# Optimization experiments

Hardware: AMD Instinct MI355X
Metric: run time of the kernel (lower is better)

Reference implementation:

```python
import jax, jax.numpy as jnp
import numpy as np

TEMPERATURE = 0.1
EPS = 1e-12


def _normalize(x):
    # torch F.normalize(dim=-1): x / max(||x||_2, eps)
    n = jnp.sqrt(jnp.sum(x * x, axis=-1, keepdims=True))
    return x / jnp.maximum(n, EPS)


def setup_inputs() -> dict:
    key = jax.random.key(0)
    k1, k2, k3 = jax.random.split(key, 3)
    b, p, d = 64, 196, 256
    return {
        "batch_tokens1": jax.random.normal(k1, (b, p, d), dtype=jnp.float32),
        "batch_tokens2": jax.random.normal(k2, (b, p, d), dtype=jnp.float32),
        "labels": jax.random.randint(k3, (b, 1), 0, 4),
        "epoch": 100,
    }


def reference(batch_tokens1, batch_tokens2, labels, epoch):
    t1 = _normalize(batch_tokens1)  # [b, p, d]
    t2 = _normalize(batch_tokens2)
    b, p, d = t1.shape

    # (b*p) x (b*p) token-wise similarity, then [b1, b2, p1, p2]
    sim = jnp.einsum('ki,mi->km', t1.reshape(b * p, d), t2.reshape(b * p, d))
    sim = sim.reshape(b, p, b, p).transpose(0, 2, 1, 3)  # [b1, b2, p1, p2]

    # max over p2 for 1->2, max over p1 for 2->1; then mean over remaining patch dim
    max12 = jnp.max(sim, axis=-1)      # [b1, b2, p1]
    idx12 = jnp.argmax(sim, axis=-1)   # [b1, b2, p1]
    sim_1_to_2 = jnp.mean(max12, axis=-1)  # [b1, b2]

    idx21 = jnp.argmax(sim, axis=-2)   # [b1, b2, p2]

    diag = jnp.arange(b)
    idx_to_keep1_2 = idx12[diag, diag]  # [b, p] (diagonal over b1==b2)
    idx_to_keep2_1 = idx21[diag, diag]  # [b, p]

    # cross-entropy of sim_1_to_2/T against targets arange(b), mean reduction
    logits = sim_1_to_2 / TEMPERATURE
    loss = jnp.mean(jax.nn.logsumexp(logits, axis=-1) - logits[diag, diag])
    return loss, idx_to_keep1_2, idx_to_keep2_1
```

## Files before the change

### kernel.cpp

```cpp
#include <hip/hip_runtime.h>
#include <math.h>

#define NB 64
#define NP 196
#define ND 256
#define NBP (NB * NP)

typedef __bf16 v8bf __attribute__((ext_vector_type(8)));
typedef float f32x16 __attribute__((ext_vector_type(16)));
typedef int v8i __attribute__((ext_vector_type(8)));

#define WS_T1Q    116736
#define WS_T2Q    3328000
#define WS_PARTS  7522304
#define WS_NEED   7923712

__device__ __forceinline__ unsigned int fmono(float v) {
    unsigned int u = __float_as_uint(v);
    return (u & 0x80000000u) ? ~u : (u | 0x80000000u);
}
__device__ __forceinline__ unsigned long long packVI(float v, int idx) {
    return ((unsigned long long)fmono(v) << 32) | (unsigned int)(~idx);
}

__device__ __forceinline__ v8i mkop(int4 lo, int4 hi) {
    v8i r;
    r[0] = lo.x; r[1] = lo.y; r[2] = lo.z; r[3] = lo.w;
    r[4] = hi.x; r[5] = hi.y; r[6] = hi.z; r[7] = hi.w;
    return r;
}


__global__ __launch_bounds__(256)
void filip_prep8(const float* __restrict__ t1, const float* __restrict__ t2,
                 float* __restrict__ inv1, float* __restrict__ inv2,
                 float* __restrict__ sim12,
                 char* __restrict__ t1q, char* __restrict__ t2q) {
    const int tid = threadIdx.x;
    if (blockIdx.x == 0) {
        float4 z = make_float4(0.f, 0.f, 0.f, 0.f);
        float4* s4 = reinterpret_cast<float4*>(sim12);
        #pragma unroll
        for (int j = 0; j < 4; ++j) s4[tid * 4 + j] = z;
    }
    int id = blockIdx.x * 4 + (tid >> 6);
    int L = tid & 63;
    int chunk = L >> 4, hi = (L >> 3) & 1, half = (L >> 2) & 1, j0 = (L & 3) * 4;
    if (id < NBP) {
        const float* src = t1 + (size_t)id * ND;
        float4 v = reinterpret_cast<const float4*>(src)[L];
        float ss = v.x * v.x + v.y * v.y + v.z * v.z + v.w * v.w;
        #pragma unroll
        for (int off = 32; off > 0; off >>= 1) ss += __shfl_xor(ss, off, 64);
        float inv = 1.0f / fmaxf(sqrtf(ss), 1e-12f);
        if (L == 0) inv1[id] = inv;
        int w0 = __builtin_amdgcn_cvt_pk_fp8_f32(v.x * inv, v.y * inv, 0, false);
        int w  = __builtin_amdgcn_cvt_pk_fp8_f32(v.z * inv, v.w * inv, w0, true);
        int t = id >> 7, r = id & 127;
        *reinterpret_cast<int*>(t1q + (size_t)t * 32768 + chunk * 8192 + hi * 4096
                                + half * 2048 + r * 16 + j0) = w;
    } else {
        int pid = id - NBP;
        int b2 = pid >> 8, c = pid & 255;
        char* dst = t2q + (size_t)b2 * 65536 + chunk * 16384 + hi * 8192
                    + half * 4096 + c * 16 + j0;
        if (c < NP) {
            const float* src = t2 + (size_t)(b2 * NP + c) * ND;
            float4 v = reinterpret_cast<const float4*>(src)[L];
            float ss = v.x * v.x + v.y * v.y + v.z * v.z + v.w * v.w;
            #pragma unroll
            for (int off = 32; off > 0; off >>= 1) ss += __shfl_xor(ss, off, 64);
            float inv = 1.0f / fmaxf(sqrtf(ss), 1e-12f);
            if (L == 0) inv2[b2 * NP + c] = inv;
            int w0 = __builtin_amdgcn_cvt_pk_fp8_f32(v.x * inv, v.y * inv, 0, false);
            int w  = __builtin_amdgcn_cvt_pk_fp8_f32(v.z * inv, v.w * inv, w0, true);
            *reinterpret_cast<int*>(dst) = w;
        } else {
            *reinterpret_cast<int*>(dst) = 0;
        }
    }
}

#define BM 128
#define BN 256

#define LOADA(TOFF)                                                          \
    _Pragma("unroll")                                                        \
    for (int c = 0; c < 4; ++c)                                              \
        _Pragma("unroll")                                                    \
        for (int mt = 0; mt < 2; ++mt) {                                     \
            const char* p = Ag + (TOFF) + c * 8192 + mt * 512;               \
            int4 lo = *reinterpret_cast<const int4*>(p);                     \
            int4 h4 = *reinterpret_cast<const int4*>(p + 2048);              \
            aA[c][mt] = mkop(lo, h4);                                        \
        }

#define ZEROACC                                                              \
    _Pragma("unroll")                                                        \
    for (int mt = 0; mt < 2; ++mt)                                           \
        _Pragma("unroll")                                                    \
        for (int nt = 0; nt < 4; ++nt)                                       \
            _Pragma("unroll")                                                \
            for (int r = 0; r < 16; ++r) acc[mt][nt][r] = 0.0f;

#define KLOOP                                                                \
    __builtin_amdgcn_s_setprio(1);                                           \
    _Pragma("unroll")                                                        \
    for (int c = 0; c < 4; ++c) {                                            \
        v8i bfr[4];                                                          \
        _Pragma("unroll")                                                    \
        for (int nt = 0; nt < 4; ++nt) {                                     \
            const char* p = Bl + c * 16384 + nt * 512;                       \
            int4 lo = *reinterpret_cast<const int4*>(p);                     \
            int4 h4 = *reinterpret_cast<const int4*>(p + 4096);              \
            bfr[nt] = mkop(lo, h4);                                          \
        }                                                                    \
        _Pragma("unroll")                                                    \
        for (int mt = 0; mt < 2; ++mt)                                       \
            _Pragma("unroll")                                                \
            for (int nt = 0; nt < 4; ++nt)                                   \
                acc[mt][nt] = __builtin_amdgcn_mfma_scale_f32_32x32x64_f8f6f4(\
                    aA[c][mt], bfr[nt], acc[mt][nt], 0, 0, 0, 127u, 0, 127u);\
    }                                                                        \
    __builtin_amdgcn_s_setprio(0);

#define FOLDRM(RM)                                                           \
    _Pragma("unroll")                                                        \
    for (int mt = 0; mt < 2; ++mt)                                           \
        _Pragma("unroll")                                                    \
        for (int r = 0; r < 16; ++r)                                         \
            RM[mt][r] = fmaxf(fmaxf(acc[mt][0][r], acc[mt][1][r]),           \
                              fmaxf(acc[mt][2][r], acc[mt][3][r]));

#define EPILOG(RM, BROW)                                                     \
    _Pragma("unroll")                                                        \
    for (int mt = 0; mt < 2; ++mt) {                                         \
        _Pragma("unroll")                                                    \
        for (int r = 0; r < 16; ++r) {                                       \
            int row = wr * 64 + mt * 32 + (r & 3) + 8 * (r >> 2) + 4 * hi;   \
            pmx[row][wc * 32 + ln] = RM[mt][r];                              \
        }                                                                    \
    }                                                                        \
    __syncthreads();                                                         \
    if (tid < BM) {                                                          \
        const float4* prow = reinterpret_cast<const float4*>(pmx[tid]);      \
        float m = -3.0e38f;                                                  \
        _Pragma("unroll")                                                    \
        for (int j = 0; j < 16; ++j) {                                       \
            float4 v = prow[j];                                              \
            m = fmaxf(m, fmaxf(fmaxf(v.x, v.y), fmaxf(v.z, v.w)));           \
        }                                                                    \
        int grow = (BROW) * BM + tid;                                        \
        int b1 = grow / NP;                                                  \
        int fb = ((BROW) * BM) / NP;                                         \
        float v0 = (b1 == fb) ? m : 0.0f;                                    \
        float v1 = (b1 != fb) ? m : 0.0f;                                    \
        _Pragma("unroll")                                                    \
        for (int off = 1; off < 64; off <<= 1) {                             \
            v0 += __shfl_xor(v0, off, 64);                                   \
            v1 += __shfl_xor(v1, off, 64);                                   \
        }                                                                    \
        if (lane == 0) {                                                     \
            atomicAdd(&sim12[fb * NB + b2], v0);                             \
            int lb = ((BROW) * BM + BM - 1) / NP;                            \
            if (lb != fb) atomicAdd(&sim12[lb * NB + b2], v1);               \
        }                                                                    \
    }                                                                        \
    __syncthreads();

__global__ __launch_bounds__(256, 2)
void filip_mega(const char* __restrict__ t1q, const char* __restrict__ t2q,
                float* __restrict__ sim12,
                const float* __restrict__ t1, const float* __restrict__ t2,
                const float* __restrict__ inv1, const float* __restrict__ inv2,
                unsigned long long* __restrict__ parts,
                float* __restrict__ out)
{
    __shared__ __align__(16) char smem[65536];
    const int bid = blockIdx.x;
    const int tid = threadIdx.x;

    if (bid >= 256) {
        int n = bid - 256;
        int x = n & 7, local = n >> 3;
        const int pairT = local >> 3;
        const int b2    = x * 8 + (local & 7);

        const int lane = tid & 63, wave = tid >> 6;
        const int wr = wave >> 1, wc = wave & 1;
        const int ln = lane & 31, hi = lane >> 5;

        const char* Ag = t1q + (size_t)(pairT * 2) * 32768
                       + hi * 4096 + (wr * 64 + ln) * 16;
        const char* Bg = t2q + (size_t)b2 * 65536;

        v8i aA[4][2];
        LOADA(0)

        #pragma unroll
        for (int i = 0; i < 16; ++i) {
            *reinterpret_cast<ulonglong2*>(smem + i * 4096 + tid * 16) =
                *reinterpret_cast<const ulonglong2*>(Bg + i * 4096 + tid * 16);
        }

        f32x16 acc[2][4];
        ZEROACC
        __syncthreads();

        const char* Bl = smem + hi * 8192 + wc * 2048 + ln * 16;
        float rm0[2][16], rm1[2][16];

        KLOOP
        FOLDRM(rm0)

        LOADA(32768)
        ZEROACC
        KLOOP
        FOLDRM(rm1)

        __syncthreads();

        float (*pmx)[68] = reinterpret_cast<float (*)[68]>(smem);
        EPILOG(rm0, pairT * 2)
        EPILOG(rm1, pairT * 2 + 1)
        return;
    }

    {
        const int q = bid & 3;
        const int b = bid >> 2;
        const int r0 = q * 49;
        const int tx = tid & 15, ty = tid >> 4;

        float* As = reinterpret_cast<float*>(smem);
        float* Bs = As + 2176;
        unsigned long long* colP = reinterpret_cast<unsigned long long*>(smem);

        const float* Ap = t1 + (size_t)b * NP * ND;
        const float* Bp = t2 + (size_t)b * NP * ND;
        const float* ia = inv1 + b * NP;
        const float* ib = inv2 + b * NP;

        float acc[4][4][4];
        #pragma unroll
        for (int i = 0; i < 4; ++i)
            #pragma unroll
            for (int j = 0; j < 4; ++j)
                #pragma unroll
                for (int l = 0; l < 4; ++l) acc[i][j][l] = 0.0f;

        for (int kc = 0; kc < 8; ++kc) {
            __syncthreads();
            #pragma unroll
            for (int i = 0; i < 2; ++i) {
                int f4 = tid + 256 * i;
                int row = f4 >> 3, k4 = f4 & 7;
                float4 v = make_float4(0.f, 0.f, 0.f, 0.f);
                if (row < 49) {
                    v = *reinterpret_cast<const float4*>(Ap + (size_t)(r0 + row) * ND + kc * 32 + 4 * k4);
                    float s = ia[r0 + row];
                    v.x *= s; v.y *= s; v.z *= s; v.w *= s;
                }
                As[(4 * k4 + 0) * 68 + row] = v.x;
                As[(4 * k4 + 1) * 68 + row] = v.y;
                As[(4 * k4 + 2) * 68 + row] = v.z;
                As[(4 * k4 + 3) * 68 + row] = v.w;
            }
            #pragma unroll
            for (int i = 0; i < 8; ++i) {
                int f4 = tid + 256 * i;
                int col = f4 >> 3, k4 = f4 & 7;
                float4 v = make_float4(0.f, 0.f, 0.f, 0.f);
                if (col < NP) {
                    v = *reinterpret_cast<const float4*>(Bp + (size_t)col * ND + kc * 32 + 4 * k4);
                    float s = ib[col];
                    v.x *= s; v.y *= s; v.z *= s; v.w *= s;
                }
                Bs[(4 * k4 + 0) * 260 + col] = v.x;
                Bs[(4 * k4 + 1) * 260 + col] = v.y;
                Bs[(4 * k4 + 2) * 260 + col] = v.z;
                Bs[(4 * k4 + 3) * 260 + col] = v.w;
            }
            __syncthreads();
            #pragma unroll 4
            for (int k = 0; k < 32; ++k) {
                float a0 = As[k * 68 + 4 * ty + 0];
                float a1 = As[k * 68 + 4 * ty + 1];
                float a2 = As[k * 68 + 4 * ty + 2];
                float a3 = As[k * 68 + 4 * ty + 3];
                float4 bq[4];
                #pragma unroll
                for (int j = 0; j < 4; ++j)
                    bq[j] = *reinterpret_cast<const float4*>(&Bs[k * 260 + 4 * tx + 64 * j]);
                #pragma unroll
                for (int j = 0; j < 4; ++j) {
                    acc[0][j][0] = fmaf(a0, bq[j].x, acc[0][j][0]);
                    acc[0][j][1] = fmaf(a0, bq[j].y, acc[0][j][1]);
                    acc[0][j][2] = fmaf(a0, bq[j].z, acc[0][j][2]);
                    acc[0][j][3] = fmaf(a0, bq[j].w, acc[0][j][3]);
                    acc[1][j][0] = fmaf(a1, bq[j].x, acc[1][j][0]);
                    acc[1][j][1] = fmaf(a1, bq[j].y, acc[1][j][1]);
                    acc[1][j][2] = fmaf(a1, bq[j].z, acc[1][j][2]);
                    acc[1][j][3] = fmaf(a1, bq[j].w, acc[1][j][3]);
                    acc[2][j][0] = fmaf(a2, bq[j].x, acc[2][j][0]);
                    acc[2][j][1] = fmaf(a2, bq[j].y, acc[2][j][1]);
                    acc[2][j][2] = fmaf(a2, bq[j].z, acc[2][j][2]);
                    acc[2][j][3] = fmaf(a2, bq[j].w, acc[2][j][3]);
                    acc[3][j][0] = fmaf(a3, bq[j].x, acc[3][j][0]);
                    acc[3][j][1] = fmaf(a3, bq[j].y, acc[3][j][1]);
                    acc[3][j][2] = fmaf(a3, bq[j].z, acc[3][j][2]);
                    acc[3][j][3] = fmaf(a3, bq[j].w, acc[3][j][3]);
                }
            }
        }

        #pragma unroll
        for (int i = 0; i < 4; ++i) {
            unsigned long long best = 0ull;
            #pragma unroll
            for (int j = 0; j < 4; ++j)
                #pragma unroll
                for (int l = 0; l < 4; ++l) {
                    int c = 64 * j + 4 * tx + l;
                    if (c < NP) {
                        unsigned long long p = packVI(acc[i][j][l], c);
                        if (p > best) best = p;
                    }
                }
            #pragma unroll
            for (int off = 1; off < 16; off <<= 1) {
                unsigned long long o = __shfl_xor(best, off, 16);
                if (o > best) best = o;
            }
            int rl = 4 * ty + i;
            if (tx == 0 && rl < 49)
                out[1 + b * NP + r0 + rl] = (float)(unsigned int)(~best);
        }

        __syncthreads();
        #pragma unroll
        for (int j = 0; j < 4; ++j)
            #pragma unroll
            for (int l = 0; l < 4; ++l) {
                unsigned long long best = 0ull;
                #pragma unroll
                for (int i = 0; i < 4; ++i) {
                    int rl = 4 * ty + i;
                    if (rl < 49) {
                        unsigned long long p = packVI(acc[i][j][l], r0 + rl);
                        if (p > best) best = p;
                    }
                }
                colP[ty * 256 + 64 * j + 4 * tx + l] = best;
            }
        __syncthreads();
        {
            unsigned long long best = 0ull;
            #pragma unroll
            for (int y = 0; y < 16; ++y) {
                unsigned long long o = colP[y * 256 + tid];
                if (o > best) best = o;
            }
            if (tid < NP) parts[(b * 4 + q) * NP + tid] = best;
        }
    }
}

__global__ void filip_finloss(const unsigned long long* __restrict__ parts,
                              const float* __restrict__ sim12,
                              float* __restrict__ out) {
    if (blockIdx.x < 49) {
        int id = blockIdx.x * 256 + threadIdx.x;
        int b = id / NP, c = id - b * NP;
        unsigned long long best = 0ull;
        #pragma unroll
        for (int qq = 0; qq < 4; ++qq) {
            unsigned long long o = parts[(b * 4 + qq) * NP + c];
            if (o > best) best = o;
        }
        out[1 + NBP + id] = (float)(unsigned int)(~best);
    } else if (threadIdx.x < 64) {
        int i = threadIdx.x;
        const float SC = 10.0f / 196.0f;
        const float* row = sim12 + i * NB;
        float mx = -3.0e38f;
        for (int j = 0; j < NB; ++j) mx = fmaxf(mx, row[j] * SC);
        float s = 0.0f;
        for (int j = 0; j < NB; ++j) s += expf(row[j] * SC - mx);
        float lse = mx + logf(s);
        float li = lse - row[i] * SC;
        #pragma unroll
        for (int off = 32; off > 0; off >>= 1)
            li += __shfl_xor(li, off, 64);
        if (i == 0) out[0] = li / 64.0f;
    }
}

__global__ void filip_norms(const float* __restrict__ t1,
                            const float* __restrict__ t2,
                            float* __restrict__ inv1,
                            float* __restrict__ inv2,
                            float* __restrict__ sim12) {
    int row = blockIdx.x;
    int lane = threadIdx.x;
    if (row < NB) sim12[row * NB + lane] = 0.0f;
    const float* src; float* dst; int r;
    if (row < NBP) { src = t1; dst = inv1; r = row; }
    else           { src = t2; dst = inv2; r = row - NBP; }
    float4 v = reinterpret_cast<const float4*>(src + (size_t)r * ND)[lane];
    float ss = v.x * v.x + v.y * v.y + v.z * v.z + v.w * v.w;
    #pragma unroll
    for (int off = 32; off > 0; off >>= 1)
        ss += __shfl_xor(ss, off, 64);
    if (lane == 0)
        dst[r] = 1.0f / fmaxf(sqrtf(ss), 1e-12f);
}

__device__ __forceinline__ v8bf cvt8(float4 a, float4 b, float s) {
    v8bf v;
    v[0] = (__bf16)(a.x * s); v[1] = (__bf16)(a.y * s);
    v[2] = (__bf16)(a.z * s); v[3] = (__bf16)(a.w * s);
    v[4] = (__bf16)(b.x * s); v[5] = (__bf16)(b.y * s);
    v[6] = (__bf16)(b.z * s); v[7] = (__bf16)(b.w * s);
    return v;
}

#define BKF 64
__global__ __launch_bounds__(256, 2)
void filip_mfma(const float* __restrict__ t1, const float* __restrict__ t2,
                const float* __restrict__ inv1, const float* __restrict__ inv2,
                float* __restrict__ sim12)
{
    __shared__ unsigned short Asb[BM * BKF];
    __shared__ unsigned short Bsb[BN * BKF];
    __shared__ float rmx[2][BM];

    const int bRow = blockIdx.x;
    const int b2   = blockIdx.y;
    const int tid  = threadIdx.x;
    const int lane = tid & 63, wave = tid >> 6;
    const int wr = wave >> 1, wc = wave & 1;
    const int ln = lane & 31, hi = lane >> 5;

    const float* Abase = t1 + (size_t)bRow * BM * ND;
    const float* Bbase = t2 + (size_t)b2 * NP * ND;

    f32x16 acc[2][4];
    #pragma unroll
    for (int mt = 0; mt < 2; ++mt)
        #pragma unroll
        for (int nt = 0; nt < 4; ++nt)
            #pragma unroll
            for (int r = 0; r < 16; ++r) acc[mt][nt][r] = 0.0f;

    for (int kc = 0; kc < 4; ++kc) {
        __syncthreads();
        #pragma unroll
        for (int i = 0; i < 4; ++i) {
            int flat = (i * 256 + tid) * 8;
            int r = flat >> 6, k0 = flat & 63;
            const float* gp = Abase + (size_t)r * ND + kc * BKF + k0;
            float4 f0 = *reinterpret_cast<const float4*>(gp);
            float4 f1 = *reinterpret_cast<const float4*>(gp + 4);
            float s = inv1[bRow * BM + r];
            v8bf v = cvt8(f0, f1, s);
            int off = r * 128 + ((k0 * 2) ^ ((r & 7) << 4));
            *reinterpret_cast<v8bf*>(reinterpret_cast<char*>(Asb) + off) = v;
        }
        #pragma unroll
        for (int i = 0; i < 8; ++i) {
            int flat = (i * 256 + tid) * 8;
            int r = flat >> 6, k0 = flat & 63;
            v8bf v;
            if (r < NP) {
                const float* gp = Bbase + (size_t)r * ND + kc * BKF + k0;
                float4 f0 = *reinterpret_cast<const float4*>(gp);
                float4 f1 = *reinterpret_cast<const float4*>(gp + 4);
                float s = inv2[b2 * NP + r];
                v = cvt8(f0, f1, s);
            } else {
                #pragma unroll
                for (int j = 0; j < 8; ++j) v[j] = (__bf16)0.0f;
            }
            int off = r * 128 + ((k0 * 2) ^ ((r & 7) << 4));
            *reinterpret_cast<v8bf*>(reinterpret_cast<char*>(Bsb) + off) = v;
        }
        __syncthreads();
        #pragma unroll
        for (int ks = 0; ks < 4; ++ks) {
            const int kb = ks * 32 + hi * 16;
            v8bf af[2], bfr[4];
            #pragma unroll
            for (int mt = 0; mt < 2; ++mt) {
                int r = wr * 64 + mt * 32 + ln;
                af[mt] = *reinterpret_cast<const v8bf*>(
                    reinterpret_cast<const char*>(Asb) + r * 128 + (kb ^ ((r & 7) << 4)));
            }
            #pragma unroll
            for (int nt = 0; nt < 4; ++nt) {
                int c = wc * 128 + nt * 32 + ln;
                bfr[nt] = *reinterpret_cast<const v8bf*>(
                    reinterpret_cast<const char*>(Bsb) + c * 128 + (kb ^ ((c & 7) << 4)));
            }
            #pragma unroll
            for (int mt = 0; mt < 2; ++mt)
                #pragma unroll
                for (int nt = 0; nt < 4; ++nt)
                    acc[mt][nt] = __builtin_amdgcn_mfma_f32_32x32x16_bf16(
                        af[mt], bfr[nt], acc[mt][nt], 0, 0, 0);
        }
    }

    #pragma unroll
    for (int mt = 0; mt < 2; ++mt) {
        float t[16];
        #pragma unroll
        for (int r = 0; r < 16; ++r) {
            float m = fmaxf(fmaxf(acc[mt][0][r], acc[mt][1][r]),
                            fmaxf(acc[mt][2][r], acc[mt][3][r]));
            #pragma unroll
            for (int off = 1; off <= 16; off <<= 1)
                m = fmaxf(m, __shfl_xor(m, off, 64));
            t[r] = m;
        }
        if (ln == 0) {
            #pragma unroll
            for (int r = 0; r < 16; ++r) {
                int row = wr * 64 + mt * 32 + (r & 3) + 8 * (r >> 2) + 4 * hi;
                rmx[wc][row] = t[r];
            }
        }
    }
    __syncthreads();
    if (tid < BM) {
        float m = fmaxf(rmx[0][tid], rmx[1][tid]);
        int grow = bRow * BM + tid;
        int b1 = grow / NP;
        int fb = (bRow * BM) / NP;
        float v0 = (b1 == fb) ? m : 0.0f;
        float v1 = (b1 != fb) ? m : 0.0f;
        #pragma unroll
        for (int off = 1; off < 64; off <<= 1) {
            v0 += __shfl_xor(v0, off, 64);
            v1 += __shfl_xor(v1, off, 64);
        }
        if (lane == 0) {
            atomicAdd(&sim12[fb * NB + b2], v0);
            int lb = (bRow * BM + BM - 1) / NP;
            if (lb != fb) atomicAdd(&sim12[lb * NB + b2], v1);
        }
    }
}

__global__ __launch_bounds__(256)
void filip_diag(const float* __restrict__ t1, const float* __restrict__ t2,
                const float* __restrict__ inv1, const float* __restrict__ inv2,
                float* __restrict__ out)
{
    const int b = blockIdx.x;
    const int tid = threadIdx.x;
    const int tx = tid & 15, ty = tid >> 4;

    __shared__ float As2[16][209];
    __shared__ float Bs2[16][65];
    __shared__ float colV[16][65];
    __shared__ int   colI[16][65];

    const float* Ap = t1 + (size_t)b * NP * ND;
    const float* Bp = t2 + (size_t)b * NP * ND;
    const float* ia = inv1 + b * NP;
    const float* ib = inv2 + b * NP;

    float rmax[13];
    int   ridx[13];
    #pragma unroll
    for (int m = 0; m < 13; ++m) { rmax[m] = -3.0e38f; ridx[m] = 1 << 30; }

    for (int tile = 0; tile < 4; ++tile) {
        float acc[13][4];
        #pragma unroll
        for (int m = 0; m < 13; ++m)
            #pragma unroll
            for (int n = 0; n < 4; ++n) acc[m][n] = 0.0f;

        for (int kk = 0; kk < 16; ++kk) {
            __syncthreads();
            #pragma unroll
            for (int i = 0; i < 13; ++i) {
                int e = tid + 256 * i;
                int p1 = e >> 4, k = e & 15;
                float v = 0.0f;
                if (p1 < NP) v = Ap[p1 * ND + kk * 16 + k] * ia[p1];
                As2[k][p1] = v;
            }
            #pragma unroll
            for (int i = 0; i < 4; ++i) {
                int e = tid + 256 * i;
                int pl = e >> 4, k = e & 15;
                int p2 = tile * 64 + pl;
                float v = 0.0f;
                if (p2 < NP) v = Bp[p2 * ND + kk * 16 + k] * ib[p2];
                Bs2[k][pl] = v;
            }
            __syncthreads();
            #pragma unroll 4
            for (int k = 0; k < 16; ++k) {
                float a[13], bq[4];
                #pragma unroll
                for (int m = 0; m < 13; ++m) a[m] = As2[k][ty + 16 * m];
                #pragma unroll
                for (int n = 0; n < 4; ++n) bq[n] = Bs2[k][tx + 16 * n];
                #pragma unroll
                for (int m = 0; m < 13; ++m)
                    #pragma unroll
                    for (int n = 0; n < 4; ++n)
                        acc[m][n] = fmaf(a[m], bq[n], acc[m][n]);
            }
        }

        #pragma unroll
        for (int n = 0; n < 4; ++n) {
            int c = tile * 64 + tx + 16 * n;
            if (c < NP) {
                #pragma unroll
                for (int m = 0; m < 13; ++m) {
                    float v = acc[m][n];
                    if (v > rmax[m] || (v == rmax[m] && c < ridx[m])) {
                        rmax[m] = v; ridx[m] = c;
                    }
                }
            }
        }

        #pragma unroll
        for (int n = 0; n < 4; ++n) {
            float bv = -3.0e38f; int bi = 1 << 30;
            #pragma unroll
            for (int m = 0; m < 13; ++m) {
                int row = ty + 16 * m;
                if (row < NP) {
                    float v = acc[m][n];
                    if (v > bv || (v == bv && row < bi)) { bv = v; bi = row; }
                }
            }
            colV[ty][tx + 16 * n] = bv;
            colI[ty][tx + 16 * n] = bi;
        }
        __syncthreads();
        if (tid < 64) {
            int c = tile * 64 + tid;
            if (c < NP) {
                float bv = -3.0e38f; int bi = 1 << 30;
                #pragma unroll
                for (int y = 0; y < 16; ++y) {
                    float v = colV[y][tid]; int i2 = colI[y][tid];
                    if (v > bv || (v == bv && i2 < bi)) { bv = v; bi = i2; }
                }
                out[1 + NBP + b * NP + c] = (float)bi;
            }
        }
        __syncthreads();
    }

    #pragma unroll
    for (int m = 0; m < 13; ++m) {
        float v = rmax[m]; int ix = ridx[m];
        #pragma unroll
        for (int off = 1; off < 16; off <<= 1) {
            float ov = __shfl_xor(v, off, 16);
            int   oi = __shfl_xor(ix, off, 16);
            if (ov > v || (ov == v && oi < ix)) { v = ov; ix = oi; }
        }
        rmax[m] = v; ridx[m] = ix;
    }
    if (tx == 0) {
        #pragma unroll
        for (int m = 0; m < 13; ++m) {
            int row = ty + 16 * m;
            if (row < NP) out[1 + b * NP + row] = (float)ridx[m];
        }
    }
}

__global__ void filip_loss(const float* __restrict__ sim12,
                           float* __restrict__ out) {
    int i = threadIdx.x;
    const float SC = 10.0f / 196.0f;
    const float* row = sim12 + i * NB;
    float mx = -3.0e38f;
    for (int j = 0; j < NB; ++j) mx = fmaxf(mx, row[j] * SC);
    float s = 0.0f;
    for (int j = 0; j < NB; ++j) s += expf(row[j] * SC - mx);
    float lse = mx + logf(s);
    float li = lse - row[i] * SC;
    #pragma unroll
    for (int off = 32; off > 0; off >>= 1)
        li += __shfl_xor(li, off, 64);
    if (i == 0) out[0] = li / 64.0f;
}

extern "C" void kernel_launch(void* const* d_in, const int* in_sizes, int n_in,
                              void* d_out, int out_size, void* d_ws, size_t ws_size,
                              hipStream_t stream) {
    const float* t1 = (const float*)d_in[0];
    const float* t2 = (const float*)d_in[1];
    float* out = (float*)d_out;
    float* ws  = (float*)d_ws;

    float* inv1  = ws;
    float* inv2  = ws + NBP;
    float* sim12 = ws + 2 * NBP;

    if (ws_size >= (size_t)WS_NEED) {
        char* t1q = (char*)d_ws + WS_T1Q;
        char* t2q = (char*)d_ws + WS_T2Q;
        unsigned long long* parts = (unsigned long long*)((char*)d_ws + WS_PARTS);

        filip_prep8<<<(NBP + NB * 256) / 4, 256, 0, stream>>>(t1, t2, inv1, inv2, sim12, t1q, t2q);
        filip_mega<<<256 + 3136, 256, 0, stream>>>(t1q, t2q, sim12, t1, t2, inv1, inv2, parts, out);
        filip_finloss<<<50, 256, 0, stream>>>(parts, sim12, out);
    } else {
        filip_norms<<<2 * NBP, 64, 0, stream>>>(t1, t2, inv1, inv2, sim12);
        filip_mfma<<<dim3(98, NB), 256, 0, stream>>>(t1, t2, inv1, inv2, sim12);
        filip_diag<<<NB, 256, 0, stream>>>(t1, t2, inv1, inv2, out);
        filip_loss<<<1, 64, 0, stream>>>(sim12, out);
    }
}
```

Baseline: 104.8 us.

## Make MFMA blocks persistent over row tiles and reduce row maxima in separate kernel

```diff
diff --git a/kernel.cpp b/kernel.cpp
--- a/kernel.cpp
+++ b/kernel.cpp
@@ -13,7 +13,8 @@
 #define WS_T1Q    116736
 #define WS_T2Q    3328000
 #define WS_PARTS  7522304
-#define WS_NEED   7923712
+#define WS_RMG    7923712
+#define WS_NEED   14346240
 
 __device__ __forceinline__ unsigned int fmono(float v) {
     unsigned int u = __float_as_uint(v);
@@ -124,56 +125,12 @@
     }                                                                        \
     __builtin_amdgcn_s_setprio(0);
 
-#define FOLDRM(RM)                                                           \
-    _Pragma("unroll")                                                        \
-    for (int mt = 0; mt < 2; ++mt)                                           \
-        _Pragma("unroll")                                                    \
-        for (int r = 0; r < 16; ++r)                                         \
-            RM[mt][r] = fmaxf(fmaxf(acc[mt][0][r], acc[mt][1][r]),           \
-                              fmaxf(acc[mt][2][r], acc[mt][3][r]));
-
-#define EPILOG(RM, BROW)                                                     \
-    _Pragma("unroll")                                                        \
-    for (int mt = 0; mt < 2; ++mt) {                                         \
-        _Pragma("unroll")                                                    \
-        for (int r = 0; r < 16; ++r) {                                       \
-            int row = wr * 64 + mt * 32 + (r & 3) + 8 * (r >> 2) + 4 * hi;   \
-            pmx[row][wc * 32 + ln] = RM[mt][r];                              \
-        }                                                                    \
-    }                                                                        \
-    __syncthreads();                                                         \
-    if (tid < BM) {                                                          \
-        const float4* prow = reinterpret_cast<const float4*>(pmx[tid]);      \
-        float m = -3.0e38f;                                                  \
-        _Pragma("unroll")                                                    \
-        for (int j = 0; j < 16; ++j) {                                       \
-            float4 v = prow[j];                                              \
-            m = fmaxf(m, fmaxf(fmaxf(v.x, v.y), fmaxf(v.z, v.w)));           \
-        }                                                                    \
-        int grow = (BROW) * BM + tid;                                        \
-        int b1 = grow / NP;                                                  \
-        int fb = ((BROW) * BM) / NP;                                         \
-        float v0 = (b1 == fb) ? m : 0.0f;                                    \
-        float v1 = (b1 != fb) ? m : 0.0f;                                    \
-        _Pragma("unroll")                                                    \
-        for (int off = 1; off < 64; off <<= 1) {                             \
-            v0 += __shfl_xor(v0, off, 64);                                   \
-            v1 += __shfl_xor(v1, off, 64);                                   \
-        }                                                                    \
-        if (lane == 0) {                                                     \
-            atomicAdd(&sim12[fb * NB + b2], v0);                             \
-            int lb = ((BROW) * BM + BM - 1) / NP;                            \
-            if (lb != fb) atomicAdd(&sim12[lb * NB + b2], v1);               \
-        }                                                                    \
-    }                                                                        \
-    __syncthreads();
-
 __global__ __launch_bounds__(256, 2)
 void filip_mega(const char* __restrict__ t1q, const char* __restrict__ t2q,
-                float* __restrict__ sim12,
                 const float* __restrict__ t1, const float* __restrict__ t2,
                 const float* __restrict__ inv1, const float* __restrict__ inv2,
                 unsigned long long* __restrict__ parts,
+                float* __restrict__ rmg,
                 float* __restrict__ out)
 {
     __shared__ __align__(16) char smem[65536];
@@ -182,47 +139,54 @@
 
     if (bid >= 256) {
         int n = bid - 256;
-        int x = n & 7, local = n >> 3;
-        const int pairT = local >> 3;
-        const int b2    = x * 8 + (local & 7);
+        int x = n & 7, j = n >> 3;
+        const int b2  = x * 8 + (j >> 4);
+        const int sub = j & 15;
 
         const int lane = tid & 63, wave = tid >> 6;
         const int wr = wave >> 1, wc = wave & 1;
         const int ln = lane & 31, hi = lane >> 5;
 
-        const char* Ag = t1q + (size_t)(pairT * 2) * 32768
-                       + hi * 4096 + (wr * 64 + ln) * 16;
+        const char* Ag = t1q + hi * 4096 + (wr * 64 + ln) * 16;
         const char* Bg = t2q + (size_t)b2 * 65536;
-
-        v8i aA[4][2];
-        LOADA(0)
 
         #pragma unroll
         for (int i = 0; i < 16; ++i) {
             *reinterpret_cast<ulonglong2*>(smem + i * 4096 + tid * 16) =
                 *reinterpret_cast<const ulonglong2*>(Bg + i * 4096 + tid * 16);
         }
-
+        __syncthreads();
+
+        const char* Bl = smem + hi * 8192 + wc * 2048 + ln * 16;
+        v8i aA[4][2];
         f32x16 acc[2][4];
-        ZEROACC
-        __syncthreads();
-
-        const char* Bl = smem + hi * 8192 + wc * 2048 + ln * 16;
-        float rm0[2][16], rm1[2][16];
-
-        KLOOP
-        FOLDRM(rm0)
-
-        LOADA(32768)
-        ZEROACC
-        KLOOP
-        FOLDRM(rm1)
-
-        __syncthreads();
-
-        float (*pmx)[68] = reinterpret_cast<float (*)[68]>(smem);
-        EPILOG(rm0, pairT * 2)
-        EPILOG(rm1, pairT * 2 + 1)
+
+        for (int t = sub; t < 98; t += 16) {
+            LOADA((size_t)t * 32768)
+            ZEROACC
+            KLOOP
+            float rm[2][16];
+            #pragma unroll
+            for (int mt = 0; mt < 2; ++mt)
+                #pragma unroll
+                for (int r = 0; r < 16; ++r) {
+                    float m = fmaxf(fmaxf(acc[mt][0][r], acc[mt][1][r]),
+                                    fmaxf(acc[mt][2][r], acc[mt][3][r]));
+                    #pragma unroll
+                    for (int off = 1; off < 32; off <<= 1)
+                        m = fmaxf(m, __shfl_xor(m, off, 64));
+                    rm[mt][r] = m;
+                }
+            if ((lane & 31) == 0) {
+                #pragma unroll
+                for (int mt = 0; mt < 2; ++mt)
+                    #pragma unroll
+                    for (int r = 0; r < 16; ++r) {
+                        int row = wr * 64 + mt * 32 + (r & 3) + 8 * (r >> 2) + 4 * hi;
+                        rmg[((size_t)t * 2 + wc) * 8192 + row * 64 + b2] = rm[mt][r];
+                    }
+            }
+        }
         return;
     }
 
@@ -364,6 +328,20 @@
             if (tid < NP) parts[(b * 4 + q) * NP + tid] = best;
         }
     }
+}
+
+__global__ void filip_rsum(const float* __restrict__ rmg,
+                           float* __restrict__ sim12) {
+    int b1 = blockIdx.x;
+    int b2 = threadIdx.x;
+    float s = 0.0f;
+    for (int p = 0; p < NP; ++p) {
+        int g = b1 * NP + p;
+        int t = g >> 7, row = g & 127;
+        const float* base = rmg + ((size_t)t * 2) * 8192 + row * 64 + b2;
+        s += fmaxf(base[0], base[8192]);
+    }
+    sim12[b1 * NB + b2] = s;
 }
 
 __global__ void filip_finloss(const unsigned long long* __restrict__ parts,
@@ -715,9 +693,11 @@
         char* t1q = (char*)d_ws + WS_T1Q;
         char* t2q = (char*)d_ws + WS_T2Q;
         unsigned long long* parts = (unsigned long long*)((char*)d_ws + WS_PARTS);
+        float* rmg = (float*)((char*)d_ws + WS_RMG);
 
         filip_prep8<<<(NBP + NB * 256) / 4, 256, 0, stream>>>(t1, t2, inv1, inv2, sim12, t1q, t2q);
-        filip_mega<<<256 + 3136, 256, 0, stream>>>(t1q, t2q, sim12, t1, t2, inv1, inv2, parts, out);
+        filip_mega<<<256 + 1024, 256, 0, stream>>>(t1q, t2q, t1, t2, inv1, inv2, parts, rmg, out);
+        filip_rsum<<<NB, NB, 0, stream>>>(rmg, sim12);
         filip_finloss<<<50, 256, 0, stream>>>(parts, sim12, out);
     } else {
         filip_norms<<<2 * NBP, 64, 0, stream>>>(t1, t2, inv1, inv2, sim12);
```

After: 197.5 us. +88.4%, slower.
